# Kernel optimization log

Measured on AMD Instinct MI355X. Metric: run time of the kernel, lower is better.

The kernel has to match this reference:

```python
import jax, jax.numpy as jnp
import numpy as np

N_P = 8192
N_T = 8192
# layer widths from GPNPolicyNet.__init__: (8,8)->(8,8)->(16,16)->(64,64)->(16,16)
DIMS = [(8, 8, 8, 8), (8, 8, 16, 16), (16, 16, 64, 64), (64, 64, 16, 16)]


def setup_inputs() -> dict:
    key = jax.random.key(0)
    ks = iter(jax.random.split(key, 64))
    inp = {
        "p": jax.random.normal(next(ks), (N_P, 8), jnp.float32),
        "t": jax.random.normal(next(ks), (N_T, 8), jnp.float32),
        # sparse-ish 0/1 Petri incidence stored dense (as in the torch module)
        "adj": (jax.random.uniform(next(ks), (N_P, N_T)) < 0.005).astype(jnp.float32),
    }
    for i, (lp_in, lt_in, lp_out, lt_out) in enumerate(DIMS, start=1):
        c = lp_in + lt_in
        sc = 1.0 / np.sqrt(c)
        inp[f"w_p{i}"] = jax.random.uniform(next(ks), (c, lp_out), jnp.float32, -sc, sc)
        inp[f"b_p{i}"] = jnp.zeros((lp_out,), jnp.float32)
        inp[f"w_t{i}"] = jax.random.uniform(next(ks), (c, lt_out), jnp.float32, -sc, sc)
        inp[f"b_t{i}"] = jnp.zeros((lt_out,), jnp.float32)
    sc = 1.0 / np.sqrt(32.0)
    inp["w_ac"] = jax.random.uniform(next(ks), (32, 1), jnp.float32, -sc, sc)
    inp["b_ac"] = jnp.zeros((1,), jnp.float32)
    return inp


def _gcpn(p, t, adj, wp, bp, wt, bt):
    agg_t = adj @ t        # [n_p, lt_in]: places gather from incident transitions
    agg_p = adj.T @ p      # [n_t, lp_in]: transitions gather from incident places
    p_out = jax.nn.relu(jnp.concatenate([p, agg_t], axis=-1) @ wp + bp)
    t_out = jax.nn.relu(jnp.concatenate([agg_p, t], axis=-1) @ wt + bt)
    return p_out, t_out


def reference(p, t, adj,
              w_p1, b_p1, w_t1, b_t1,
              w_p2, b_p2, w_t2, b_t2,
              w_p3, b_p3, w_t3, b_t3,
              w_p4, b_p4, w_t4, b_t4,
              w_ac, b_ac):
    p, t = _gcpn(p, t, adj, w_p1, b_p1, w_t1, b_t1)
    p, t = _gcpn(p, t, adj, w_p2, b_p2, w_t2, b_t2)
    p, t = _gcpn(p, t, adj, w_p3, b_p3, w_t3, b_t3)
    p, t = _gcpn(p, t, adj, w_p4, b_p4, w_t4, b_t4)
    x = jnp.concatenate([adj.T @ p, t], axis=-1)  # [n_t, 32]
    logits = (x @ w_ac + b_ac)[:, 0]              # [n_t]
    return jax.nn.softmax(logits, axis=-1)        # firing distribution over transitions
```

## Files before the change

kernel.cpp:

```cpp
#include <hip/hip_runtime.h>
#include <hip/hip_bf16.h>
#include <math.h>

#define N_NODES 8192
#define CAP 128
#define WPR 256

__global__ __launch_bounds__(256) void build_bits(const float4* __restrict__ adj4,
                                                  unsigned* __restrict__ rowBits,
                                                  unsigned* __restrict__ colBits) {
    __shared__ unsigned rb[128 * 4];
    __shared__ unsigned cb[128 * 4];
    const int tid = threadIdx.x;
    rb[tid] = 0; rb[tid + 256] = 0;
    cb[tid] = 0; cb[tid + 256] = 0;
    __syncthreads();

    const int tileR = blockIdx.x >> 6;
    const int tileC = blockIdx.x & 63;
    const int R0 = tileR * 128;
    const int C0 = tileC * 128;

    float4 v[16];
#pragma unroll
    for (int k = 0; k < 16; ++k) {
        int fi = k * 256 + tid;
        int r  = fi >> 5;
        int c4 = fi & 31;
        v[k] = adj4[(size_t)(R0 + r) * 2048 + (C0 >> 2) + c4];
    }
#pragma unroll
    for (int k = 0; k < 16; ++k) {
        int fi = k * 256 + tid;
        int r  = fi >> 5;
        int cb4 = (fi & 31) * 4;
        float vals[4] = {v[k].x, v[k].y, v[k].z, v[k].w};
        if (vals[0] != 0.f || vals[1] != 0.f || vals[2] != 0.f || vals[3] != 0.f) {
#pragma unroll
            for (int e = 0; e < 4; ++e) {
                if (vals[e] != 0.f) {
                    int c = cb4 + e;
                    atomicOr(&rb[r * 4 + (c >> 5)], 1u << (c & 31));
                    atomicOr(&cb[c * 4 + (r >> 5)], 1u << (r & 31));
                }
            }
        }
    }
    __syncthreads();
    if (tid < 128) {
        uint4 q = make_uint4(rb[tid * 4], rb[tid * 4 + 1], rb[tid * 4 + 2], rb[tid * 4 + 3]);
        *(uint4*)(rowBits + (size_t)(R0 + tid) * WPR + tileC * 4) = q;
    } else {
        int c = tid - 128;
        uint4 q = make_uint4(cb[c * 4], cb[c * 4 + 1], cb[c * 4 + 2], cb[c * 4 + 3]);
        *(uint4*)(colBits + (size_t)(C0 + c) * WPR + tileR * 4) = q;
    }
}

__global__ __launch_bounds__(256) void build_lists(const unsigned* __restrict__ rowBits,
                                                   const unsigned* __restrict__ colBits,
                                                   int* __restrict__ rowCnt, int* __restrict__ rowIdx,
                                                   int* __restrict__ colCnt, int* __restrict__ colIdx) {
    const int rl = threadIdx.x >> 6, lane = threadIdx.x & 63;
    const bool cSide = blockIdx.x >= 2048;
    const int n = (cSide ? blockIdx.x - 2048 : blockIdx.x) * 4 + rl;
    const unsigned* bits = (cSide ? colBits : rowBits) + (size_t)n * WPR;
    int* cnt = cSide ? colCnt : rowCnt;
    int* lst = (cSide ? colIdx : rowIdx) + n * CAP;

    uint4 w4 = ((const uint4*)bits)[lane];
    int pc = __popc(w4.x) + __popc(w4.y) + __popc(w4.z) + __popc(w4.w);
    int incl = pc;
    for (int d = 1; d < 64; d <<= 1) {
        int nv = __shfl_up(incl, d);
        if (lane >= d) incl += nv;
    }
    int off = incl - pc;
    int total = __shfl(incl, 63);
    unsigned wds[4] = {w4.x, w4.y, w4.z, w4.w};
    const int base = lane * 128;
#pragma unroll
    for (int w = 0; w < 4; ++w) {
        unsigned word = wds[w];
        while (word) {
            int b = __ffs(word) - 1;
            word &= word - 1;
            if (off < CAP) lst[off] = base + w * 32 + b;
            ++off;
        }
    }
    if (lane == 0) cnt[n] = total > CAP ? CAP : total;
}

template <int CI, int CO, bool RELU, bool TONLY>
__global__ __launch_bounds__(256) void layer2_k(const float* __restrict__ pIn,
                                                const float* __restrict__ tIn,
                                                const int* __restrict__ rowCnt, const int* __restrict__ rowIdx,
                                                const int* __restrict__ colCnt, const int* __restrict__ colIdx,
                                                const float* __restrict__ Wp, const float* __restrict__ Bp,
                                                const float* __restrict__ Wt, const float* __restrict__ Bt,
                                                float* __restrict__ pOut, float* __restrict__ tOut) {
    constexpr int C = 2 * CI;
    constexpr int G = 64 / CI;
    __shared__ float sW[C * CO];
    __shared__ float sB[CO];
    __shared__ float sIn[4][C];

    const int rl = threadIdx.x >> 6, lane = threadIdx.x & 63;
    const bool tSide = TONLY ? true : (blockIdx.x >= (N_NODES / 4));
    const int row = (TONLY ? blockIdx.x
                           : (tSide ? blockIdx.x - N_NODES / 4 : blockIdx.x)) * 4 + rl;

    const float* W  = tSide ? Wt : Wp;
    const float* Bv = tSide ? Bt : Bp;
    for (int k = threadIdx.x; k < C * CO; k += 256) sW[k] = W[k];
    if (threadIdx.x < CO) sB[threadIdx.x] = Bv[threadIdx.x];

    const float* self_in = tSide ? tIn : pIn;
    const float* oth_in  = tSide ? pIn : tIn;
    const int* cnt  = tSide ? colCnt : rowCnt;
    const int* idxl = tSide ? colIdx : rowIdx;

    const int feat = lane & (CI - 1);
    const int grp  = lane / CI;
    int m = cnt[row];
    if (m > CAP) m = CAP;
    const int* __restrict__ lst = idxl + row * CAP;

    const int len = (m + G - 1) / G;
    const int s0 = grp * len;
    const int s1 = min(s0 + len, m);
    float acc = 0.f;
    int s = s0;
    for (; s + 8 <= s1; s += 8) {
        int j0 = lst[s],     j1 = lst[s + 1], j2 = lst[s + 2], j3 = lst[s + 3];
        int j4 = lst[s + 4], j5 = lst[s + 5], j6 = lst[s + 6], j7 = lst[s + 7];
        float a0 = oth_in[j0 * CI + feat];
        float a1 = oth_in[j1 * CI + feat];
        float a2 = oth_in[j2 * CI + feat];
        float a3 = oth_in[j3 * CI + feat];
        float a4 = oth_in[j4 * CI + feat];
        float a5 = oth_in[j5 * CI + feat];
        float a6 = oth_in[j6 * CI + feat];
        float a7 = oth_in[j7 * CI + feat];
        acc += ((a0 + a1) + (a2 + a3)) + ((a4 + a5) + (a6 + a7));
    }
    for (; s + 4 <= s1; s += 4) {
        int j0 = lst[s], j1 = lst[s + 1], j2 = lst[s + 2], j3 = lst[s + 3];
        float a0 = oth_in[j0 * CI + feat];
        float a1 = oth_in[j1 * CI + feat];
        float a2 = oth_in[j2 * CI + feat];
        float a3 = oth_in[j3 * CI + feat];
        acc += (a0 + a1) + (a2 + a3);
    }
    for (; s < s1; ++s) acc += oth_in[lst[s] * CI + feat];
#pragma unroll
    for (int off = 32; off >= CI; off >>= 1) acc += __shfl_down(acc, off);

    if (lane < CI) {
        const int aggOff  = tSide ? 0 : CI;
        const int selfOff = tSide ? CI : 0;
        sIn[rl][aggOff + lane]  = acc;
        sIn[rl][selfOff + lane] = self_in[row * CI + lane];
    }
    __syncthreads();
    if (lane < CO) {
        float o = sB[lane];
#pragma unroll
        for (int k = 0; k < C; ++k) o += sIn[rl][k] * sW[k * CO + lane];
        if (RELU) o = fmaxf(o, 0.f);
        (tSide ? tOut : pOut)[row * CO + lane] = o;
    }
}

__global__ __launch_bounds__(1024) void softmax_k(const float4* __restrict__ logits4,
                                                  float4* __restrict__ out4) {
    __shared__ float red[1024];
    float4 a = logits4[threadIdx.x];
    float4 b = logits4[threadIdx.x + 1024];
    float mx = fmaxf(fmaxf(fmaxf(a.x, a.y), fmaxf(a.z, a.w)),
                     fmaxf(fmaxf(b.x, b.y), fmaxf(b.z, b.w)));
    red[threadIdx.x] = mx;
    __syncthreads();
    for (int s = 512; s > 0; s >>= 1) {
        if (threadIdx.x < s) red[threadIdx.x] = fmaxf(red[threadIdx.x], red[threadIdx.x + s]);
        __syncthreads();
    }
    mx = red[0];
    __syncthreads();
    a.x = __expf(a.x - mx); a.y = __expf(a.y - mx);
    a.z = __expf(a.z - mx); a.w = __expf(a.w - mx);
    b.x = __expf(b.x - mx); b.y = __expf(b.y - mx);
    b.z = __expf(b.z - mx); b.w = __expf(b.w - mx);
    float sum = ((a.x + a.y) + (a.z + a.w)) + ((b.x + b.y) + (b.z + b.w));
    red[threadIdx.x] = sum;
    __syncthreads();
    for (int s = 512; s > 0; s >>= 1) {
        if (threadIdx.x < s) red[threadIdx.x] += red[threadIdx.x + s];
        __syncthreads();
    }
    float inv = 1.f / red[0];
    a.x *= inv; a.y *= inv; a.z *= inv; a.w *= inv;
    b.x *= inv; b.y *= inv; b.z *= inv; b.w *= inv;
    out4[threadIdx.x] = a;
    out4[threadIdx.x + 1024] = b;
}

extern "C" void kernel_launch(void* const* d_in, const int* in_sizes, int n_in,
                              void* d_out, int out_size, void* d_ws, size_t ws_size,
                              hipStream_t stream) {
    const float* p    = (const float*)d_in[0];
    const float* t    = (const float*)d_in[1];
    const float* adj  = (const float*)d_in[2];
    const float* w_p1 = (const float*)d_in[3];
    const float* b_p1 = (const float*)d_in[4];
    const float* w_t1 = (const float*)d_in[5];
    const float* b_t1 = (const float*)d_in[6];
    const float* w_p2 = (const float*)d_in[7];
    const float* b_p2 = (const float*)d_in[8];
    const float* w_t2 = (const float*)d_in[9];
    const float* b_t2 = (const float*)d_in[10];
    const float* w_p3 = (const float*)d_in[11];
    const float* b_p3 = (const float*)d_in[12];
    const float* w_t3 = (const float*)d_in[13];
    const float* b_t3 = (const float*)d_in[14];
    const float* w_p4 = (const float*)d_in[15];
    const float* b_p4 = (const float*)d_in[16];
    const float* w_t4 = (const float*)d_in[17];
    const float* b_t4 = (const float*)d_in[18];
    const float* w_ac = (const float*)d_in[19];
    const float* b_ac = (const float*)d_in[20];

    char* ws = (char*)d_ws;
    int*      rowCnt  = (int*)(ws);
    int*      colCnt  = (int*)(ws + 32768);
    int*      rowIdx  = (int*)(ws + 65536);
    int*      colIdx  = (int*)(ws + 65536 + 4194304);
    unsigned* rowBits = (unsigned*)(ws + 8454144);
    unsigned* colBits = (unsigned*)(ws + 8454144 + 8388608);
    float* pA     = (float*)(ws + 8454144);
    float* pB     = (float*)(ws + 8454144 + 2097152);
    float* tA     = (float*)(ws + 8454144 + 2 * 2097152);
    float* tB     = (float*)(ws + 8454144 + 3 * 2097152);
    float* logits = (float*)(ws + 8454144 + 8388608);

    build_bits<<<4096, 256, 0, stream>>>((const float4*)adj, rowBits, colBits);
    build_lists<<<4096, 256, 0, stream>>>(rowBits, colBits, rowCnt, rowIdx, colCnt, colIdx);

    const int LG2 = N_NODES / 2;

    layer2_k<8, 8, true, false><<<LG2, 256, 0, stream>>>(
        p, t, rowCnt, rowIdx, colCnt, colIdx, w_p1, b_p1, w_t1, b_t1, pA, tA);
    layer2_k<8, 16, true, false><<<LG2, 256, 0, stream>>>(
        pA, tA, rowCnt, rowIdx, colCnt, colIdx, w_p2, b_p2, w_t2, b_t2, pB, tB);
    layer2_k<16, 64, true, false><<<LG2, 256, 0, stream>>>(
        pB, tB, rowCnt, rowIdx, colCnt, colIdx, w_p3, b_p3, w_t3, b_t3, pA, tA);
    layer2_k<64, 16, true, false><<<LG2, 256, 0, stream>>>(
        pA, tA, rowCnt, rowIdx, colCnt, colIdx, w_p4, b_p4, w_t4, b_t4, pB, tB);
    layer2_k<16, 1, false, true><<<N_NODES / 4, 256, 0, stream>>>(
        pB, tB, rowCnt, rowIdx, colCnt, colIdx, w_ac, b_ac, w_ac, b_ac, logits, logits);

    softmax_k<<<1, 1024, 0, stream>>>((const float4*)logits, (float4*)d_out);
}
```

Measured before the change: 465.7 us.

## Fuse all stages into one persistent cooperative kernel with grid barriers

Replaces the eight separate launches (bit building, list building, five layers, softmax) with one persistent cooperative kernel of 1024 blocks. Each block loops over tiles, rows and tasks, and the stages are separated by atomic-counter grid barriers. This removes per-launch overhead and launch gaps between the many small kernels. In exchange it adds barrier spin costs, a memset per call, and lower parallelism per stage. If the cooperative launch fails, the code falls back to separate launches.

```diff
diff --git a/kernel.cpp b/kernel.cpp
--- a/kernel.cpp
+++ b/kernel.cpp
@@ -1,264 +1,354 @@
 #include <hip/hip_runtime.h>
-#include <hip/hip_bf16.h>
 #include <math.h>
 
 #define N_NODES 8192
 #define CAP 128
 #define WPR 256
-
-__global__ __launch_bounds__(256) void build_bits(const float4* __restrict__ adj4,
-                                                  unsigned* __restrict__ rowBits,
-                                                  unsigned* __restrict__ colBits) {
+#define NBLK 1024
+#define NWAVE (NBLK * 4)
+
+struct Params {
+    const float4* adj4;
+    const float* p; const float* t;
+    const float* w_p1; const float* b_p1; const float* w_t1; const float* b_t1;
+    const float* w_p2; const float* b_p2; const float* w_t2; const float* b_t2;
+    const float* w_p3; const float* b_p3; const float* w_t3; const float* b_t3;
+    const float* w_p4; const float* b_p4; const float* w_t4; const float* b_t4;
+    const float* w_ac; const float* b_ac;
+    unsigned* rowBits; unsigned* colBits;
+    int* rowCnt; int* rowIdx; int* colCnt; int* colIdx;
+    float* pA; float* pB; float* tA; float* tB; float* logits;
+    unsigned* bar;
+    float4* out4;
+};
+
+__device__ __forceinline__ void gbar(unsigned* cnt) {
+    __syncthreads();
+    if (threadIdx.x == 0) {
+        __threadfence_system();
+        __hip_atomic_fetch_add(cnt, 1u, __ATOMIC_RELEASE, __HIP_MEMORY_SCOPE_AGENT);
+        while (__hip_atomic_load(cnt, __ATOMIC_ACQUIRE, __HIP_MEMORY_SCOPE_AGENT) < NBLK)
+            __builtin_amdgcn_s_sleep(8);
+        __threadfence_system();
+    }
+    __syncthreads();
+}
+
+__device__ __forceinline__ void phaseA(const Params& P, unsigned* rb, unsigned* cb) {
+    const int tid = threadIdx.x;
+#pragma unroll 1
+    for (int it = 0; it < 4; ++it) {
+        const int tile = blockIdx.x + it * NBLK;
+        rb[tid] = 0; rb[tid + 256] = 0;
+        cb[tid] = 0; cb[tid + 256] = 0;
+        __syncthreads();
+        const int tileR = tile >> 6;
+        const int tileC = tile & 63;
+        const int R0 = tileR * 128;
+        const int C0 = tileC * 128;
+
+        float4 v[16];
+#pragma unroll
+        for (int k = 0; k < 16; ++k) {
+            int fi = k * 256 + tid;
+            int r  = fi >> 5;
+            int c4 = fi & 31;
+            v[k] = P.adj4[(size_t)(R0 + r) * 2048 + (C0 >> 2) + c4];
+        }
+#pragma unroll
+        for (int k = 0; k < 16; ++k) {
+            int fi = k * 256 + tid;
+            int r  = fi >> 5;
+            int cb4 = (fi & 31) * 4;
+            float vals[4] = {v[k].x, v[k].y, v[k].z, v[k].w};
+            if (vals[0] != 0.f || vals[1] != 0.f || vals[2] != 0.f || vals[3] != 0.f) {
+#pragma unroll
+                for (int e = 0; e < 4; ++e) {
+                    if (vals[e] != 0.f) {
+                        int c = cb4 + e;
+                        atomicOr(&rb[r * 4 + (c >> 5)], 1u << (c & 31));
+                        atomicOr(&cb[c * 4 + (r >> 5)], 1u << (r & 31));
+                    }
+                }
+            }
+        }
+        __syncthreads();
+        if (tid < 128) {
+            uint4 q = make_uint4(rb[tid * 4], rb[tid * 4 + 1], rb[tid * 4 + 2], rb[tid * 4 + 3]);
+            *(uint4*)(P.rowBits + (size_t)(R0 + tid) * WPR + tileC * 4) = q;
+        } else {
+            int c = tid - 128;
+            uint4 q = make_uint4(cb[c * 4], cb[c * 4 + 1], cb[c * 4 + 2], cb[c * 4 + 3]);
+            *(uint4*)(P.colBits + (size_t)(C0 + c) * WPR + tileR * 4) = q;
+        }
+        __syncthreads();
+    }
+}
+
+__device__ __forceinline__ void phaseB(const Params& P) {
+    const int rl = threadIdx.x >> 6, lane = threadIdx.x & 63;
+    const int wg = blockIdx.x * 4 + rl;
+#pragma unroll 1
+    for (int id = wg; id < 2 * N_NODES; id += NWAVE) {
+        const bool cSide = id >= N_NODES;
+        const int n = cSide ? id - N_NODES : id;
+        const unsigned* bits = (cSide ? P.colBits : P.rowBits) + (size_t)n * WPR;
+        int* cnt = cSide ? P.colCnt : P.rowCnt;
+        int* lst = (cSide ? P.colIdx : P.rowIdx) + n * CAP;
+
+        uint4 w4 = ((const uint4*)bits)[lane];
+        int pc = __popc(w4.x) + __popc(w4.y) + __popc(w4.z) + __popc(w4.w);
+        int incl = pc;
+        for (int d = 1; d < 64; d <<= 1) {
+            int nv = __shfl_up(incl, d);
+            if (lane >= d) incl += nv;
+        }
+        int off = incl - pc;
+        int total = __shfl(incl, 63);
+        unsigned wds[4] = {w4.x, w4.y, w4.z, w4.w};
+        const int base = lane * 128;
+#pragma unroll
+        for (int w = 0; w < 4; ++w) {
+            unsigned word = wds[w];
+            while (word) {
+                int b = __ffs(word) - 1;
+                word &= word - 1;
+                if (off < CAP) lst[off] = base + w * 32 + b;
+                ++off;
+            }
+        }
+        if (lane == 0) cnt[n] = total > CAP ? CAP : total;
+    }
+}
+
+template <int CI, int CO, bool RELU, bool TONLY>
+__device__ __forceinline__ void layer_step(
+    const Params& P,
+    const float* __restrict__ pIn, const float* __restrict__ tIn,
+    const float* __restrict__ Wp, const float* __restrict__ Bp,
+    const float* __restrict__ Wt, const float* __restrict__ Bt,
+    float* __restrict__ pOut, float* __restrict__ tOut,
+    float* sWp, float* sWt, float* sBp, float* sBt, float (*sIn)[128])
+{
+    constexpr int C = 2 * CI;
+    constexpr int G = 64 / CI;
+    for (int k = threadIdx.x; k < C * CO; k += 256) { sWp[k] = Wp[k]; sWt[k] = Wt[k]; }
+    if (threadIdx.x < CO) { sBp[threadIdx.x] = Bp[threadIdx.x]; sBt[threadIdx.x] = Bt[threadIdx.x]; }
+    __syncthreads();
+
+    const int rl = threadIdx.x >> 6, lane = threadIdx.x & 63;
+    const int wg = blockIdx.x * 4 + rl;
+    const int feat = lane & (CI - 1);
+    const int grp = lane / CI;
+    constexpr int NT = TONLY ? N_NODES : 2 * N_NODES;
+
+#pragma unroll 1
+    for (int task = wg; task < NT; task += NWAVE) {
+        const bool tSide = TONLY ? true : (task >= N_NODES);
+        const int row = TONLY ? task : (tSide ? task - N_NODES : task);
+        const float* self_in = tSide ? tIn : pIn;
+        const float* oth_in  = tSide ? pIn : tIn;
+        const int* cnt  = tSide ? P.colCnt : P.rowCnt;
+        const int* idxl = tSide ? P.colIdx : P.rowIdx;
+        const float* sW  = tSide ? sWt : sWp;
+        const float* sBv = tSide ? sBt : sBp;
+
+        int m = cnt[row];
+        if (m > CAP) m = CAP;
+        const int* __restrict__ lst = idxl + row * CAP;
+
+        const int len = (m + G - 1) / G;
+        const int s0 = grp * len;
+        const int s1 = min(s0 + len, m);
+        float acc = 0.f;
+        int s = s0;
+        for (; s + 8 <= s1; s += 8) {
+            int j0 = lst[s],     j1 = lst[s + 1], j2 = lst[s + 2], j3 = lst[s + 3];
+            int j4 = lst[s + 4], j5 = lst[s + 5], j6 = lst[s + 6], j7 = lst[s + 7];
+            float a0 = oth_in[j0 * CI + feat];
+            float a1 = oth_in[j1 * CI + feat];
+            float a2 = oth_in[j2 * CI + feat];
+            float a3 = oth_in[j3 * CI + feat];
+            float a4 = oth_in[j4 * CI + feat];
+            float a5 = oth_in[j5 * CI + feat];
+            float a6 = oth_in[j6 * CI + feat];
+            float a7 = oth_in[j7 * CI + feat];
+            acc += ((a0 + a1) + (a2 + a3)) + ((a4 + a5) + (a6 + a7));
+        }
+        for (; s + 4 <= s1; s += 4) {
+            int j0 = lst[s], j1 = lst[s + 1], j2 = lst[s + 2], j3 = lst[s + 3];
+            float a0 = oth_in[j0 * CI + feat];
+            float a1 = oth_in[j1 * CI + feat];
+            float a2 = oth_in[j2 * CI + feat];
+            float a3 = oth_in[j3 * CI + feat];
+            acc += (a0 + a1) + (a2 + a3);
+        }
+        for (; s < s1; ++s) acc += oth_in[lst[s] * CI + feat];
+#pragma unroll
+        for (int off = 32; off >= CI; off >>= 1) acc += __shfl_down(acc, off);
+
+        if (lane < CI) {
+            const int aggOff  = tSide ? 0 : CI;
+            const int selfOff = tSide ? CI : 0;
+            sIn[rl][aggOff + lane]  = acc;
+            sIn[rl][selfOff + lane] = self_in[row * CI + lane];
+        }
+        __syncthreads();
+        if (lane < CO) {
+            float o = sBv[lane];
+#pragma unroll
+            for (int k = 0; k < C; ++k) o += sIn[rl][k] * sW[k * CO + lane];
+            if (RELU) o = fmaxf(o, 0.f);
+            (tSide ? tOut : pOut)[row * CO + lane] = o;
+        }
+        __syncthreads();
+    }
+}
+
+__device__ __forceinline__ void softmax_dev(const Params& P, float* red) {
+    const int tid = threadIdx.x;
+    const float4* lg4 = (const float4*)P.logits;
+    float4 va[8];
+    float mx = -INFINITY;
+#pragma unroll
+    for (int k = 0; k < 8; ++k) {
+        va[k] = lg4[tid + 256 * k];
+        mx = fmaxf(mx, fmaxf(fmaxf(va[k].x, va[k].y), fmaxf(va[k].z, va[k].w)));
+    }
+    red[tid] = mx;
+    __syncthreads();
+    for (int s2 = 128; s2 > 0; s2 >>= 1) {
+        if (tid < s2) red[tid] = fmaxf(red[tid], red[tid + s2]);
+        __syncthreads();
+    }
+    mx = red[0];
+    __syncthreads();
+    float sum = 0.f;
+#pragma unroll
+    for (int k = 0; k < 8; ++k) {
+        va[k].x = __expf(va[k].x - mx); va[k].y = __expf(va[k].y - mx);
+        va[k].z = __expf(va[k].z - mx); va[k].w = __expf(va[k].w - mx);
+        sum += (va[k].x + va[k].y) + (va[k].z + va[k].w);
+    }
+    red[tid] = sum;
+    __syncthreads();
+    for (int s2 = 128; s2 > 0; s2 >>= 1) {
+        if (tid < s2) red[tid] += red[tid + s2];
+        __syncthreads();
+    }
+    float inv = 1.f / red[0];
+#pragma unroll
+    for (int k = 0; k < 8; ++k) {
+        va[k].x *= inv; va[k].y *= inv; va[k].z *= inv; va[k].w *= inv;
+        P.out4[tid + 256 * k] = va[k];
+    }
+}
+
+__global__ __launch_bounds__(256, 4) void gcn_fused(Params P) {
     __shared__ unsigned rb[128 * 4];
     __shared__ unsigned cb[128 * 4];
-    const int tid = threadIdx.x;
-    rb[tid] = 0; rb[tid + 256] = 0;
-    cb[tid] = 0; cb[tid + 256] = 0;
-    __syncthreads();
-
-    const int tileR = blockIdx.x >> 6;
-    const int tileC = blockIdx.x & 63;
-    const int R0 = tileR * 128;
-    const int C0 = tileC * 128;
-
-    float4 v[16];
-#pragma unroll
-    for (int k = 0; k < 16; ++k) {
-        int fi = k * 256 + tid;
-        int r  = fi >> 5;
-        int c4 = fi & 31;
-        v[k] = adj4[(size_t)(R0 + r) * 2048 + (C0 >> 2) + c4];
-    }
-#pragma unroll
-    for (int k = 0; k < 16; ++k) {
-        int fi = k * 256 + tid;
-        int r  = fi >> 5;
-        int cb4 = (fi & 31) * 4;
-        float vals[4] = {v[k].x, v[k].y, v[k].z, v[k].w};
-        if (vals[0] != 0.f || vals[1] != 0.f || vals[2] != 0.f || vals[3] != 0.f) {
-#pragma unroll
-            for (int e = 0; e < 4; ++e) {
-                if (vals[e] != 0.f) {
-                    int c = cb4 + e;
-                    atomicOr(&rb[r * 4 + (c >> 5)], 1u << (c & 31));
-                    atomicOr(&cb[c * 4 + (r >> 5)], 1u << (r & 31));
-                }
-            }
-        }
-    }
-    __syncthreads();
-    if (tid < 128) {
-        uint4 q = make_uint4(rb[tid * 4], rb[tid * 4 + 1], rb[tid * 4 + 2], rb[tid * 4 + 3]);
-        *(uint4*)(rowBits + (size_t)(R0 + tid) * WPR + tileC * 4) = q;
-    } else {
-        int c = tid - 128;
-        uint4 q = make_uint4(cb[c * 4], cb[c * 4 + 1], cb[c * 4 + 2], cb[c * 4 + 3]);
-        *(uint4*)(colBits + (size_t)(C0 + c) * WPR + tileR * 4) = q;
-    }
-}
-
-__global__ __launch_bounds__(256) void build_lists(const unsigned* __restrict__ rowBits,
-                                                   const unsigned* __restrict__ colBits,
-                                                   int* __restrict__ rowCnt, int* __restrict__ rowIdx,
-                                                   int* __restrict__ colCnt, int* __restrict__ colIdx) {
-    const int rl = threadIdx.x >> 6, lane = threadIdx.x & 63;
-    const bool cSide = blockIdx.x >= 2048;
-    const int n = (cSide ? blockIdx.x - 2048 : blockIdx.x) * 4 + rl;
-    const unsigned* bits = (cSide ? colBits : rowBits) + (size_t)n * WPR;
-    int* cnt = cSide ? colCnt : rowCnt;
-    int* lst = (cSide ? colIdx : rowIdx) + n * CAP;
-
-    uint4 w4 = ((const uint4*)bits)[lane];
-    int pc = __popc(w4.x) + __popc(w4.y) + __popc(w4.z) + __popc(w4.w);
-    int incl = pc;
-    for (int d = 1; d < 64; d <<= 1) {
-        int nv = __shfl_up(incl, d);
-        if (lane >= d) incl += nv;
-    }
-    int off = incl - pc;
-    int total = __shfl(incl, 63);
-    unsigned wds[4] = {w4.x, w4.y, w4.z, w4.w};
-    const int base = lane * 128;
-#pragma unroll
-    for (int w = 0; w < 4; ++w) {
-        unsigned word = wds[w];
-        while (word) {
-            int b = __ffs(word) - 1;
-            word &= word - 1;
-            if (off < CAP) lst[off] = base + w * 32 + b;
-            ++off;
-        }
-    }
-    if (lane == 0) cnt[n] = total > CAP ? CAP : total;
-}
+    __shared__ float sW[2][2048];
+    __shared__ float sB[2][64];
+    __shared__ float sIn[4][128];
+    __shared__ float red[256];
+
+    phaseA(P, rb, cb);
+    gbar(&P.bar[0]);
+    phaseB(P);
+    gbar(&P.bar[1]);
+    layer_step<8, 8, true, false>(P, P.p, P.t, P.w_p1, P.b_p1, P.w_t1, P.b_t1,
+                                  P.pA, P.tA, sW[0], sW[1], sB[0], sB[1], sIn);
+    gbar(&P.bar[2]);
+    layer_step<8, 16, true, false>(P, P.pA, P.tA, P.w_p2, P.b_p2, P.w_t2, P.b_t2,
+                                   P.pB, P.tB, sW[0], sW[1], sB[0], sB[1], sIn);
+    gbar(&P.bar[3]);
+    layer_step<16, 64, true, false>(P, P.pB, P.tB, P.w_p3, P.b_p3, P.w_t3, P.b_t3,
+                                    P.pA, P.tA, sW[0], sW[1], sB[0], sB[1], sIn);
+    gbar(&P.bar[4]);
+    layer_step<64, 16, true, false>(P, P.pA, P.tA, P.w_p4, P.b_p4, P.w_t4, P.b_t4,
+                                    P.pB, P.tB, sW[0], sW[1], sB[0], sB[1], sIn);
+    gbar(&P.bar[5]);
+    layer_step<16, 1, false, true>(P, P.pB, P.tB, P.w_ac, P.b_ac, P.w_ac, P.b_ac,
+                                   P.logits, P.logits, sW[0], sW[1], sB[0], sB[1], sIn);
+    gbar(&P.bar[6]);
+    if (blockIdx.x == 0) softmax_dev(P, red);
+}
+
+__global__ __launch_bounds__(256) void phaseA_k(Params P) {
+    __shared__ unsigned rb[128 * 4];
+    __shared__ unsigned cb[128 * 4];
+    phaseA(P, rb, cb);
+}
+__global__ __launch_bounds__(256) void phaseB_k(Params P) { phaseB(P); }
 
 template <int CI, int CO, bool RELU, bool TONLY>
-__global__ __launch_bounds__(256) void layer2_k(const float* __restrict__ pIn,
-                                                const float* __restrict__ tIn,
-                                                const int* __restrict__ rowCnt, const int* __restrict__ rowIdx,
-                                                const int* __restrict__ colCnt, const int* __restrict__ colIdx,
-                                                const float* __restrict__ Wp, const float* __restrict__ Bp,
-                                                const float* __restrict__ Wt, const float* __restrict__ Bt,
-                                                float* __restrict__ pOut, float* __restrict__ tOut) {
-    constexpr int C = 2 * CI;
-    constexpr int G = 64 / CI;
-    __shared__ float sW[C * CO];
-    __shared__ float sB[CO];
-    __shared__ float sIn[4][C];
-
-    const int rl = threadIdx.x >> 6, lane = threadIdx.x & 63;
-    const bool tSide = TONLY ? true : (blockIdx.x >= (N_NODES / 4));
-    const int row = (TONLY ? blockIdx.x
-                           : (tSide ? blockIdx.x - N_NODES / 4 : blockIdx.x)) * 4 + rl;
-
-    const float* W  = tSide ? Wt : Wp;
-    const float* Bv = tSide ? Bt : Bp;
-    for (int k = threadIdx.x; k < C * CO; k += 256) sW[k] = W[k];
-    if (threadIdx.x < CO) sB[threadIdx.x] = Bv[threadIdx.x];
-
-    const float* self_in = tSide ? tIn : pIn;
-    const float* oth_in  = tSide ? pIn : tIn;
-    const int* cnt  = tSide ? colCnt : rowCnt;
-    const int* idxl = tSide ? colIdx : rowIdx;
-
-    const int feat = lane & (CI - 1);
-    const int grp  = lane / CI;
-    int m = cnt[row];
-    if (m > CAP) m = CAP;
-    const int* __restrict__ lst = idxl + row * CAP;
-
-    const int len = (m + G - 1) / G;
-    const int s0 = grp * len;
-    const int s1 = min(s0 + len, m);
-    float acc = 0.f;
-    int s = s0;
-    for (; s + 8 <= s1; s += 8) {
-        int j0 = lst[s],     j1 = lst[s + 1], j2 = lst[s + 2], j3 = lst[s + 3];
-        int j4 = lst[s + 4], j5 = lst[s + 5], j6 = lst[s + 6], j7 = lst[s + 7];
-        float a0 = oth_in[j0 * CI + feat];
-        float a1 = oth_in[j1 * CI + feat];
-        float a2 = oth_in[j2 * CI + feat];
-        float a3 = oth_in[j3 * CI + feat];
-        float a4 = oth_in[j4 * CI + feat];
-        float a5 = oth_in[j5 * CI + feat];
-        float a6 = oth_in[j6 * CI + feat];
-        float a7 = oth_in[j7 * CI + feat];
-        acc += ((a0 + a1) + (a2 + a3)) + ((a4 + a5) + (a6 + a7));
-    }
-    for (; s + 4 <= s1; s += 4) {
-        int j0 = lst[s], j1 = lst[s + 1], j2 = lst[s + 2], j3 = lst[s + 3];
-        float a0 = oth_in[j0 * CI + feat];
-        float a1 = oth_in[j1 * CI + feat];
-        float a2 = oth_in[j2 * CI + feat];
-        float a3 = oth_in[j3 * CI + feat];
-        acc += (a0 + a1) + (a2 + a3);
-    }
-    for (; s < s1; ++s) acc += oth_in[lst[s] * CI + feat];
-#pragma unroll
-    for (int off = 32; off >= CI; off >>= 1) acc += __shfl_down(acc, off);
-
-    if (lane < CI) {
-        const int aggOff  = tSide ? 0 : CI;
-        const int selfOff = tSide ? CI : 0;
-        sIn[rl][aggOff + lane]  = acc;
-        sIn[rl][selfOff + lane] = self_in[row * CI + lane];
-    }
-    __syncthreads();
-    if (lane < CO) {
-        float o = sB[lane];
-#pragma unroll
-        for (int k = 0; k < C; ++k) o += sIn[rl][k] * sW[k * CO + lane];
-        if (RELU) o = fmaxf(o, 0.f);
-        (tSide ? tOut : pOut)[row * CO + lane] = o;
-    }
-}
-
-__global__ __launch_bounds__(1024) void softmax_k(const float4* __restrict__ logits4,
-                                                  float4* __restrict__ out4) {
-    __shared__ float red[1024];
-    float4 a = logits4[threadIdx.x];
-    float4 b = logits4[threadIdx.x + 1024];
-    float mx = fmaxf(fmaxf(fmaxf(a.x, a.y), fmaxf(a.z, a.w)),
-                     fmaxf(fmaxf(b.x, b.y), fmaxf(b.z, b.w)));
-    red[threadIdx.x] = mx;
-    __syncthreads();
-    for (int s = 512; s > 0; s >>= 1) {
-        if (threadIdx.x < s) red[threadIdx.x] = fmaxf(red[threadIdx.x], red[threadIdx.x + s]);
-        __syncthreads();
-    }
-    mx = red[0];
-    __syncthreads();
-    a.x = __expf(a.x - mx); a.y = __expf(a.y - mx);
-    a.z = __expf(a.z - mx); a.w = __expf(a.w - mx);
-    b.x = __expf(b.x - mx); b.y = __expf(b.y - mx);
-    b.z = __expf(b.z - mx); b.w = __expf(b.w - mx);
-    float sum = ((a.x + a.y) + (a.z + a.w)) + ((b.x + b.y) + (b.z + b.w));
-    red[threadIdx.x] = sum;
-    __syncthreads();
-    for (int s = 512; s > 0; s >>= 1) {
-        if (threadIdx.x < s) red[threadIdx.x] += red[threadIdx.x + s];
-        __syncthreads();
-    }
-    float inv = 1.f / red[0];
-    a.x *= inv; a.y *= inv; a.z *= inv; a.w *= inv;
-    b.x *= inv; b.y *= inv; b.z *= inv; b.w *= inv;
-    out4[threadIdx.x] = a;
-    out4[threadIdx.x + 1024] = b;
+__global__ __launch_bounds__(256) void layer_k(Params P,
+    const float* pIn, const float* tIn,
+    const float* Wp, const float* Bp, const float* Wt, const float* Bt,
+    float* pOut, float* tOut)
+{
+    __shared__ float sW[2][2048];
+    __shared__ float sB[2][64];
+    __shared__ float sIn[4][128];
+    layer_step<CI, CO, RELU, TONLY>(P, pIn, tIn, Wp, Bp, Wt, Bt, pOut, tOut,
+                                    sW[0], sW[1], sB[0], sB[1], sIn);
+}
+__global__ __launch_bounds__(256) void softmax_k(Params P) {
+    __shared__ float red[256];
+    softmax_dev(P, red);
 }
 
 extern "C" void kernel_launch(void* const* d_in, const int* in_sizes, int n_in,
                               void* d_out, int out_size, void* d_ws, size_t ws_size,
                               hipStream_t stream) {
-    const float* p    = (const float*)d_in[0];
-    const float* t    = (const float*)d_in[1];
-    const float* adj  = (const float*)d_in[2];
-    const float* w_p1 = (const float*)d_in[3];
-    const float* b_p1 = (const float*)d_in[4];
-    const float* w_t1 = (const float*)d_in[5];
-    const float* b_t1 = (const float*)d_in[6];
-    const float* w_p2 = (const float*)d_in[7];
-    const float* b_p2 = (const float*)d_in[8];
-    const float* w_t2 = (const float*)d_in[9];
-    const float* b_t2 = (const float*)d_in[10];
-    const float* w_p3 = (const float*)d_in[11];
-    const float* b_p3 = (const float*)d_in[12];
-    const float* w_t3 = (const float*)d_in[13];
-    const float* b_t3 = (const float*)d_in[14];
-    const float* w_p4 = (const float*)d_in[15];
-    const float* b_p4 = (const float*)d_in[16];
-    const float* w_t4 = (const float*)d_in[17];
-    const float* b_t4 = (const float*)d_in[18];
-    const float* w_ac = (const float*)d_in[19];
-    const float* b_ac = (const float*)d_in[20];
-
     char* ws = (char*)d_ws;
-    int*      rowCnt  = (int*)(ws);
-    int*      colCnt  = (int*)(ws + 32768);
-    int*      rowIdx  = (int*)(ws + 65536);
-    int*      colIdx  = (int*)(ws + 65536 + 4194304);
-    unsigned* rowBits = (unsigned*)(ws + 8454144);
-    unsigned* colBits = (unsigned*)(ws + 8454144 + 8388608);
-    float* pA     = (float*)(ws + 8454144);
-    float* pB     = (float*)(ws + 8454144 + 2097152);
-    float* tA     = (float*)(ws + 8454144 + 2 * 2097152);
-    float* tB     = (float*)(ws + 8454144 + 3 * 2097152);
-    float* logits = (float*)(ws + 8454144 + 8388608);
-
-    build_bits<<<4096, 256, 0, stream>>>((const float4*)adj, rowBits, colBits);
-    build_lists<<<4096, 256, 0, stream>>>(rowBits, colBits, rowCnt, rowIdx, colCnt, colIdx);
-
-    const int LG2 = N_NODES / 2;
-
-    layer2_k<8, 8, true, false><<<LG2, 256, 0, stream>>>(
-        p, t, rowCnt, rowIdx, colCnt, colIdx, w_p1, b_p1, w_t1, b_t1, pA, tA);
-    layer2_k<8, 16, true, false><<<LG2, 256, 0, stream>>>(
-        pA, tA, rowCnt, rowIdx, colCnt, colIdx, w_p2, b_p2, w_t2, b_t2, pB, tB);
-    layer2_k<16, 64, true, false><<<LG2, 256, 0, stream>>>(
-        pB, tB, rowCnt, rowIdx, colCnt, colIdx, w_p3, b_p3, w_t3, b_t3, pA, tA);
-    layer2_k<64, 16, true, false><<<LG2, 256, 0, stream>>>(
-        pA, tA, rowCnt, rowIdx, colCnt, colIdx, w_p4, b_p4, w_t4, b_t4, pB, tB);
-    layer2_k<16, 1, false, true><<<N_NODES / 4, 256, 0, stream>>>(
-        pB, tB, rowCnt, rowIdx, colCnt, colIdx, w_ac, b_ac, w_ac, b_ac, logits, logits);
-
-    softmax_k<<<1, 1024, 0, stream>>>((const float4*)logits, (float4*)d_out);
-}
+    Params prm;
+    prm.adj4 = (const float4*)d_in[2];
+    prm.p    = (const float*)d_in[0];
+    prm.t    = (const float*)d_in[1];
+    prm.w_p1 = (const float*)d_in[3];  prm.b_p1 = (const float*)d_in[4];
+    prm.w_t1 = (const float*)d_in[5];  prm.b_t1 = (const float*)d_in[6];
+    prm.w_p2 = (const float*)d_in[7];  prm.b_p2 = (const float*)d_in[8];
+    prm.w_t2 = (const float*)d_in[9];  prm.b_t2 = (const float*)d_in[10];
+    prm.w_p3 = (const float*)d_in[11]; prm.b_p3 = (const float*)d_in[12];
+    prm.w_t3 = (const float*)d_in[13]; prm.b_t3 = (const float*)d_in[14];
+    prm.w_p4 = (const float*)d_in[15]; prm.b_p4 = (const float*)d_in[16];
+    prm.w_t4 = (const float*)d_in[17]; prm.b_t4 = (const float*)d_in[18];
+    prm.w_ac = (const float*)d_in[19]; prm.b_ac = (const float*)d_in[20];
+
+    const size_t MB = 1024 * 1024;
+    prm.rowCnt  = (int*)(ws);
+    prm.colCnt  = (int*)(ws + 32768);
+    prm.bar     = (unsigned*)(ws + 65536);
+    prm.rowIdx  = (int*)(ws + 1 * MB);
+    prm.colIdx  = (int*)(ws + 5 * MB);
+    prm.rowBits = (unsigned*)(ws + 16 * MB);
+    prm.colBits = (unsigned*)(ws + 24 * MB);
+    prm.pA      = (float*)(ws + 32 * MB);
+    prm.pB      = (float*)(ws + 34 * MB);
+    prm.tA      = (float*)(ws + 36 * MB);
+    prm.tB      = (float*)(ws + 38 * MB);
+    prm.logits  = (float*)(ws + 40 * MB);
+    prm.out4    = (float4*)d_out;
+
+    hipMemsetAsync(prm.bar, 0, 256, stream);
+
+    void* args[] = { (void*)&prm };
+    hipError_t e = hipLaunchCooperativeKernel(reinterpret_cast<void*>(&gcn_fused),
+                                              dim3(NBLK), dim3(256), args, 0, stream);
+    if (e != hipSuccess) {
+        phaseA_k<<<NBLK, 256, 0, stream>>>(prm);
+        phaseB_k<<<NBLK, 256, 0, stream>>>(prm);
+        layer_k<8, 8, true, false><<<NBLK, 256, 0, stream>>>(
+            prm, prm.p, prm.t, prm.w_p1, prm.b_p1, prm.w_t1, prm.b_t1, prm.pA, prm.tA);
+        layer_k<8, 16, true, false><<<NBLK, 256, 0, stream>>>(
+            prm, prm.pA, prm.tA, prm.w_p2, prm.b_p2, prm.w_t2, prm.b_t2, prm.pB, prm.tB);
+        layer_k<16, 64, true, false><<<NBLK, 256, 0, stream>>>(
+            prm, prm.pB, prm.tB, prm.w_p3, prm.b_p3, prm.w_t3, prm.b_t3, prm.pA, prm.tA);
+        layer_k<64, 16, true, false><<<NBLK, 256, 0, stream>>>(
+            prm, prm.pA, prm.tA, prm.w_p4, prm.b_p4, prm.w_t4, prm.b_t4, prm.pB, prm.tB);
+        layer_k<16, 1, false, true><<<NBLK, 256, 0, stream>>>(
+            prm, prm.pB, prm.tB, prm.w_ac, prm.b_ac, prm.w_ac, prm.b_ac, prm.logits, prm.logits);
+        softmax_k<<<1, 256, 0, stream>>>(prm);
+    }
+}
```

Measured after the change: 1.726 ms. 3.71x slower.
